# Performance work log

Hardware: AMD Instinct MI355X
Metric: run time of the kernel (lower is better)

The kernel has to match this reference:

```python
import jax, jax.numpy as jnp
import numpy as np

B, S, D = 4, 2048, 1024
N_NEURONS, K = 512, 8
N_BASIS, R = 32, 512
N_HEADS = 8
D_HEAD = R // N_HEADS


def setup_inputs() -> dict:
    key = jax.random.key(0)
    ks = jax.random.split(key, 8)
    x = jax.random.normal(ks[0], (B, S, D), dtype=jnp.float32)
    W_router = jax.random.normal(ks[1], (N_NEURONS, D), dtype=jnp.float32) / np.sqrt(D)
    recipe_Q = jax.random.normal(ks[2], (N_NEURONS, N_BASIS), dtype=jnp.float32)
    recipe_K = jax.random.normal(ks[3], (N_NEURONS, N_BASIS), dtype=jnp.float32)
    recipe_V = jax.random.normal(ks[4], (N_NEURONS, N_BASIS), dtype=jnp.float32)
    # orthonormal basis: QR of random [D, R] per basis slot (buffer, not trained)
    raw = jax.random.normal(ks[5], (N_BASIS, D, R), dtype=jnp.float32)
    basis = jax.vmap(lambda m: jnp.linalg.qr(m)[0])(raw)  # [N_BASIS, D, R]
    W_o = jax.random.normal(ks[6], (D, R), dtype=jnp.float32) / np.sqrt(R)
    mask = jnp.tril(jnp.ones((S, S), dtype=jnp.int32))[None, None]  # [1,1,S,S] causal
    mask = jnp.broadcast_to(mask, (B, 1, S, S))
    return {"x": x, "W_router": W_router, "recipe_Q": recipe_Q, "recipe_K": recipe_K,
            "recipe_V": recipe_V, "basis": basis, "W_o": W_o, "mask": mask}


def reference(x, W_router, recipe_Q, recipe_K, recipe_V, basis, W_o, mask):
    # routing: pick top-k neurons per token
    scores = jnp.einsum('bsd,nd->bsn', x, W_router)            # [B,S,N_NEURONS]
    topk_scores, topk_idx = jax.lax.top_k(scores, K)            # [B,S,K]
    weights = jax.nn.softmax(topk_scores, axis=-1)              # [B,S,K]

    def token_recipe(recipe):
        g = recipe[topk_idx]                                    # [B,S,K,N_BASIS]
        r = jnp.einsum('bskn,bsk->bsn', g, weights)             # [B,S,N_BASIS]
        return jax.nn.softmax(r, axis=-1)

    tQ = token_recipe(recipe_Q)
    tK = token_recipe(recipe_K)
    tV = token_recipe(recipe_V)

    # shared basis projection of x, reused for Q/K/V (same math as
    # W = einsum('bsn,ndr->bsdr'); Q = einsum('bsd,bsdr->bsr'))
    P = jnp.einsum('bsd,ndr->bsnr', x, basis)                   # [B,S,N_BASIS,R]
    Q = jnp.einsum('bsnr,bsn->bsr', P, tQ)
    Kt = jnp.einsum('bsnr,bsn->bsr', P, tK)
    V = jnp.einsum('bsnr,bsn->bsr', P, tV)

    def heads(t):
        return t.reshape(B, S, N_HEADS, D_HEAD).transpose(0, 2, 1, 3)  # [B,H,S,dh]

    Qh, Kh, Vh = heads(Q), heads(Kt), heads(V)
    attn = jnp.einsum('bhqd,bhkd->bhqk', Qh, Kh) / np.sqrt(D_HEAD)
    attn = jnp.where(mask == 0, jnp.float32(-1e30), attn)
    attn = jax.nn.softmax(attn, axis=-1)                        # dropout p: eval/no-op
    out = jnp.einsum('bhqk,bhkd->bhqd', attn, Vh)
    out = out.transpose(0, 2, 1, 3).reshape(B, S, R)
    attn_out = jnp.einsum('bsr,dr->bsd', out, W_o)
    return attn_out, topk_idx, weights
```

## Files before the change

kernel.cpp:

```cpp
#include <hip/hip_runtime.h>
#include <math.h>
#include <stdint.h>


typedef __attribute__((ext_vector_type(4))) float f32x4;
typedef __attribute__((ext_vector_type(8))) short s16x8;
typedef __attribute__((ext_vector_type(4))) short s16x4;
typedef __attribute__((ext_vector_type(4))) int i32x4;
typedef __attribute__((ext_vector_type(8))) int i32x8;

#define DEV __device__ __forceinline__

DEV short f2bf(float f){
  union { float f; unsigned u; } c; c.f = f;
  unsigned u = c.u;
  unsigned r = (u + 0x7fffu + ((u >> 16) & 1u)) >> 16;
  return (short)r;
}
DEV float bf2f(short s){
  union { unsigned u; float f; } c; c.u = ((unsigned)(unsigned short)s) << 16;
  return c.f;
}
DEV unsigned char f2e4m3(float f){
  union { float f; unsigned u; } c; c.f = f;
  unsigned u = c.u;
  unsigned sign = (u >> 24) & 0x80u;
  unsigned a = u & 0x7fffffffu;
  if (a >= 0x43e00000u) return (unsigned char)(sign | 0x7Eu);
  if (a < 0x3c800000u){
    union { unsigned u; float f; } d; d.u = a;
    int q = (int)(d.f * 512.0f + 0.5f);
    return (unsigned char)(sign | (unsigned)q);
  }
  unsigned m = a & 0x7fffffu;
  unsigned e = (a >> 23) - 120u;
  unsigned keep = m >> 20;
  unsigned rest = m & 0xFFFFFu;
  if (rest > 0x80000u || (rest == 0x80000u && (keep & 1u))){
    keep++;
    if (keep == 8u){ keep = 0; e++; }
  }
  if (e >= 16u || (e == 15u && keep == 7u)) return (unsigned char)(sign | 0x7Eu);
  return (unsigned char)(sign | (e << 3) | keep);
}

typedef __attribute__((address_space(3))) void lds_vt;
typedef const __attribute__((address_space(1))) void g_vt;
DEV void gload16(const void* g, void* lds){
  __builtin_amdgcn_global_load_lds((g_vt*)g, (lds_vt*)lds, 16, 0, 0);
}

DEV int gslot(int c){ return (c < 4) ? (c << 1) : (((c - 4) << 1) + 1); }

__global__ void k_conv_w(const float* __restrict__ Wo, const float* __restrict__ Wrt,
                         short* __restrict__ Wob, short* __restrict__ Wrtb){
  int i = blockIdx.x*256 + threadIdx.x;
  const float* src = (i < 131072) ? Wo : Wrt;
  short* dst = (i < 131072) ? Wob : Wrtb;
  int j = (i < 131072) ? i : (i - 131072);
  float4 v = ((const float4*)src)[j];
  s16x4 o; o[0]=f2bf(v.x); o[1]=f2bf(v.y); o[2]=f2bf(v.z); o[3]=f2bf(v.w);
  ((s16x4*)dst)[j] = o;
}

__global__ void k_conv_x(const float* __restrict__ in, short* __restrict__ Xb, char* __restrict__ Xf8){
  int t = blockIdx.x*256 + threadIdx.x;
  size_t d = (size_t)t * 16;
  const float4* s = (const float4*)(in + d);
  float vals[16];
  #pragma unroll
  for (int q=0;q<4;q++){ float4 v = s[q]; vals[q*4]=v.x; vals[q*4+1]=v.y; vals[q*4+2]=v.z; vals[q*4+3]=v.w; }
  s16x8 ob0, ob1;
  unsigned long long v0 = 0, v1 = 0;
  #pragma unroll
  for (int e=0;e<8;e++){
    ob0[e] = f2bf(vals[e]);
    ob1[e] = f2bf(vals[8+e]);
    v0 |= ((unsigned long long)f2e4m3(vals[e]))   << (8*e);
    v1 |= ((unsigned long long)f2e4m3(vals[8+e])) << (8*e);
  }
  *(s16x8*)(Xb + d) = ob0;
  *(s16x8*)(Xb + d + 8) = ob1;
  int c = t & 7;
  char* dst = Xf8 + (d & ~(size_t)127) + (gslot(c) << 4);
  *(unsigned long long*)dst = v0;
  *(unsigned long long*)(dst + 8) = v1;
}

__global__ __launch_bounds__(256) void k_conv_basis8(const float* __restrict__ basis, char* __restrict__ B2f){
  __shared__ float tile[64][65];
  int tid = threadIdx.x;
  int r0 = blockIdx.x<<6, d0 = blockIdx.y<<6, n = blockIdx.z;
  const float* src = basis + ((size_t)n*1024 + d0)*512 + r0;
  for (int i = tid; i < 4096; i += 256){ int dd = i>>6, rr = i&63; tile[dd][rr] = src[(size_t)dd*512 + rr]; }
  __syncthreads();
  int rr = tid >> 2, j = tid & 3;
  unsigned long long v0 = 0, v1 = 0;
  #pragma unroll
  for (int e=0;e<8;e++){
    v0 |= ((unsigned long long)f2e4m3(tile[j*16+e][rr]))   << (8*e);
    v1 |= ((unsigned long long)f2e4m3(tile[j*16+8+e][rr])) << (8*e);
  }
  int c = j + ((d0 >> 4) & 4);
  char* dst = B2f + ((size_t)(r0+rr)*32 + n)*1024 + (size_t)(d0 & ~127) + (gslot(c) << 4);
  *(unsigned long long*)dst = v0;
  *(unsigned long long*)(dst + 8) = v1;
}

__global__ __launch_bounds__(256) void k_gemm_c32(
    const short* __restrict__ A, const short* __restrict__ Bt, int Kd, int Mblk,
    float* __restrict__ C, int ldc)
{
  __shared__ char smem[32768];
  short* Asm = (short*)smem;
  short* Bsm = (short*)(smem + 16384);
  int tid = threadIdx.x, lane = tid & 63, w = tid >> 6;
  int wr = w >> 1, wc = w & 1;
  int nwg = gridDim.x, bid = blockIdx.x;
  int sid = (bid & 7) * (nwg >> 3) + (bid >> 3);
  int row0 = (sid % Mblk) << 7;
  int col0 = (sid / Mblk) << 7;
  f32x4 acc[4][4];
  #pragma unroll
  for (int m=0;m<4;m++)
    #pragma unroll
    for (int nf=0;nf<4;nf++)
      #pragma unroll
      for (int e=0;e<4;e++) acc[m][nf][e] = 0.f;
  int lr8 = lane >> 3;
  int lk_sw = (((lane & 7) ^ (lane >> 3)) << 3);
  for (int k0 = 0; k0 < Kd; k0 += 64){
    #pragma unroll
    for (int i=0;i<4;i++){
      int chunk = (w<<2) + i;
      int r = (chunk<<3) + lr8;
      gload16(A  + (size_t)(row0 + r)*Kd + k0 + lk_sw, smem + chunk*1024);
      gload16(Bt + (size_t)(col0 + r)*Kd + k0 + lk_sw, smem + 16384 + chunk*1024);
    }
    __syncthreads();
    #pragma unroll
    for (int kk=0; kk<2; kk++){
      int csw = (kk*32 + ((lane>>4)<<3)) ^ ((lane & 7) << 3);
      s16x8 af[4], bfr[4];
      #pragma unroll
      for (int m=0;m<4;m++)
        af[m] = *(const s16x8*)(Asm + ((wr*64 + m*16 + (lane&15))*64 + csw));
      #pragma unroll
      for (int nf=0;nf<4;nf++)
        bfr[nf] = *(const s16x8*)(Bsm + ((wc*64 + nf*16 + (lane&15))*64 + csw));
      #pragma unroll
      for (int m=0;m<4;m++)
        #pragma unroll
        for (int nf=0;nf<4;nf++)
          acc[m][nf] = __builtin_amdgcn_mfma_f32_16x16x32_bf16(af[m], bfr[nf], acc[m][nf], 0, 0, 0);
    }
    __syncthreads();
  }
  #pragma unroll
  for (int m=0;m<4;m++)
    #pragma unroll
    for (int nf=0;nf<4;nf++)
      #pragma unroll
      for (int e=0;e<4;e++){
        int tok = wr*64 + m*16 + ((lane>>4)<<2) + e;
        int col = wc*64 + nf*16 + (lane&15);
        C[(size_t)(row0+tok)*ldc + col0 + col] = acc[m][nf][e];
      }
}

#define STAGE8(G, tileRow0, half, tkt) do{ \
  int _t = (tkt) < 7 ? (tkt) : 7; \
  char* _d = smem + ((G)==Xf8 ? 65536 : 0) + ((_t&1)*32768) + ((half)*16384) + (wid*2048); \
  const char* _s = (G) + (size_t)((tileRow0) + (half)*128 + wid*16 + (lane>>3))*1024 + (_t<<7) + (((lane&7)^(lane>>3))<<4); \
  gload16(_s, _d); \
  gload16(_s + 8192, _d + 1024); \
}while(0)

#define LD_AF8(dst, base) \
  _Pragma("unroll") \
  for (int i=0;i<4;i++){ \
    const char* _p = (base) + (wm*64 + i*16 + l15)*128; \
    i32x4* _h = (i32x4*)&dst[i]; \
    _h[0] = *(const i32x4*)(_p + ((ga0 ^ l7)<<4)); \
    _h[1] = *(const i32x4*)(_p + ((ga1 ^ l7)<<4)); \
  }

#define LD_BF8(dst, base) \
  _Pragma("unroll") \
  for (int n=0;n<2;n++){ \
    const char* _p = (base) + (wn*32 + n*16 + l15)*128; \
    i32x4* _h = (i32x4*)&dst[n]; \
    _h[0] = *(const i32x4*)(_p + ((ga0 ^ l7)<<4)); \
    _h[1] = *(const i32x4*)(_p + ((ga1 ^ l7)<<4)); \
  }

#define VMC(N) asm volatile("s_waitcnt vmcnt(" #N ")" ::: "memory")
#define PBAR() do{ __builtin_amdgcn_sched_barrier(0); __builtin_amdgcn_s_barrier(); }while(0)

#define MFMA_Q8(Q, AF, BF) do{ \
  __builtin_amdgcn_s_setprio(1); \
  _Pragma("unroll") \
  for (int i=0;i<4;i++) \
    _Pragma("unroll") \
    for (int n=0;n<2;n++) \
      acc[Q][i][n] = __builtin_amdgcn_mfma_scale_f32_16x16x128_f8f6f4( \
          AF[i], BF[n], acc[Q][i][n], 0, 0, 0, 0x7f7f7f7f, 0, 0x7f7f7f7f); \
  __builtin_amdgcn_s_setprio(0); \
}while(0)

__global__ __launch_bounds__(512, 2) void k_pgemm8(
    const char* __restrict__ B2f, const char* __restrict__ Xf8,
    const float* __restrict__ tQp, const float* __restrict__ tKp, const float* __restrict__ tVp,
    short* __restrict__ Qb, short* __restrict__ Kb, short* __restrict__ Vt)
{
  extern __shared__ char smem[];
  int tid = threadIdx.x, lane = tid & 63, wid = tid >> 6;
  int wm = wid >> 2, wn = wid & 3;
  int l15 = lane & 15, l7 = lane & 7, g16 = lane >> 4;
  int ga0 = (g16 < 2) ? (g16 << 2) : (((g16 - 2) << 2) + 1);
  int ga1 = ga0 + 2;
  int bid = blockIdx.x;
  int xcd = bid & 7, lid = bid >> 3;
  int t_tile = (xcd << 2) + (lid & 3);
  int c_tile = lid >> 2;
  int row0 = c_tile << 8;
  int col0 = t_tile << 8;

  f32x4 acc[4][4][2];
  #pragma unroll
  for (int q=0;q<4;q++)
    #pragma unroll
    for (int m=0;m<4;m++)
      #pragma unroll
      for (int n=0;n<2;n++)
        #pragma unroll
        for (int e=0;e<4;e++) acc[q][m][n][e] = 0.f;
  i32x8 af[4], bf0[2], bf1[2];

  STAGE8(B2f, row0, 0, 0);
  STAGE8(Xf8, col0, 0, 0);
  STAGE8(Xf8, col0, 1, 0);
  STAGE8(B2f, row0, 1, 0);
  VMC(4);
  PBAR();

  for (int kt = 0; kt < 8; ++kt){
    const char* Ac = smem + (kt&1)*32768;
    const char* Bc = smem + 65536 + (kt&1)*32768;
    LD_AF8(af,  Ac);
    LD_BF8(bf0, Bc);
    STAGE8(B2f, row0, 0, kt+1);
    VMC(4);
    PBAR();
    MFMA_Q8(0, af, bf0);
    LD_BF8(bf1, Bc + 16384);
    STAGE8(Xf8, col0, 0, kt+1);
    VMC(4);
    PBAR();
    MFMA_Q8(1, af, bf1);
    LD_AF8(af, Ac + 16384);
    STAGE8(Xf8, col0, 1, kt+1);
    PBAR();
    MFMA_Q8(2, af, bf0);
    STAGE8(B2f, row0, 1, kt+1);
    VMC(4);
    PBAR();
    MFMA_Q8(3, af, bf1);
  }

  VMC(0);
  __syncthreads();
  short* t16 = (short*)smem;
  for (int i = tid; i < 8192; i += 512){
    int tk = i >> 5, n = i & 31;
    t16[tk*36 + n]            = f2bf(tQp[(size_t)col0*32 + i]);
    t16[9216 + tk*36 + n]     = f2bf(tKp[(size_t)col0*32 + i]);
    t16[18432 + tk*36 + n]    = f2bf(tVp[(size_t)col0*32 + i]);
  }
  __syncthreads();
  int g4 = g16 << 2;
  #pragma unroll
  for (int rec=0; rec<3; rec++){
    const short* tb = t16 + rec*9216;
    #pragma unroll
    for (int q=0;q<4;q++){
      int rb = (row0 >> 5) + (q>>1)*4 + wm*2;
      #pragma unroll
      for (int n=0;n<2;n++){
        int tok = (q&1)*128 + wn*32 + n*16 + l15;
        s16x4 tlo = *(const s16x4*)(tb + tok*36 + g4);
        s16x4 thi = *(const s16x4*)(tb + tok*36 + 16 + g4);
        #pragma unroll
        for (int mp=0;mp<2;mp++){
          float p = 0.f;
          #pragma unroll
          for (int e=0;e<4;e++) p += acc[q][2*mp][n][e]   * bf2f(tlo[e]);
          #pragma unroll
          for (int e=0;e<4;e++) p += acc[q][2*mp+1][n][e] * bf2f(thi[e]);
          p += __shfl_xor(p, 16);
          p += __shfl_xor(p, 32);
          if (g16 == rec){
            int gtok = col0 + tok;
            int r = rb + mp;
            if (rec == 0)      Qb[(size_t)gtok*512 + r] = f2bf(p);
            else if (rec == 1) Kb[(size_t)gtok*512 + r] = f2bf(p);
            else Vt[(((size_t)(gtok>>11)*8 + (r>>6))*64 + (r&63))*2048 + (gtok&2047)] = f2bf(p);
          }
        }
      }
    }
  }
}

__global__ __launch_bounds__(64) void k_router(const float* __restrict__ scores,
    const float* __restrict__ X, const float* __restrict__ W,
    const float* __restrict__ rQ, const float* __restrict__ rK, const float* __restrict__ rV,
    float* __restrict__ tQ, float* __restrict__ tK, float* __restrict__ tV,
    float* __restrict__ oidx, float* __restrict__ ow){
  int token = blockIdx.x; int lane = threadIdx.x;
  const float* srow = scores + (size_t)token*512;
  float v[8];
  #pragma unroll
  for (int j=0;j<8;j++) v[j] = srow[lane + 64*j];
  int myidx = 0x7fffffff;
  #pragma unroll
  for (int k=0;k<16;k++){
    float bm = -INFINITY; int bi = 0x7fffffff;
    #pragma unroll
    for (int j=0;j<8;j++){ if (v[j] > bm) { bm = v[j]; bi = lane + 64*j; } }
    #pragma unroll
    for (int off=32; off>=1; off>>=1){
      float om = __shfl_xor(bm, off); int oi = __shfl_xor(bi, off);
      if (om > bm || (om == bm && oi < bi)) { bm = om; bi = oi; }
    }
    if (lane == k) myidx = bi;
    #pragma unroll
    for (int j=0;j<8;j++) if (lane + 64*j == bi) v[j] = -INFINITY;
  }
  float xr[16];
  {
    const float4* x4 = (const float4*)(X + (size_t)token*1024 + lane*16);
    #pragma unroll
    for (int q=0;q<4;q++){ float4 t = x4[q]; xr[q*4]=t.x; xr[q*4+1]=t.y; xr[q*4+2]=t.z; xr[q*4+3]=t.w; }
  }
  double myref = -1e300;
  #pragma unroll
  for (int c=0;c<16;c++){
    int nid = __shfl(myidx, c);
    const float4* w4 = (const float4*)(W + (size_t)nid*1024 + lane*16);
    double acc = 0.0;
    #pragma unroll
    for (int q=0;q<4;q++){
      float4 t = w4[q];
      acc += (double)xr[q*4]   * (double)t.x;
      acc += (double)xr[q*4+1] * (double)t.y;
      acc += (double)xr[q*4+2] * (double)t.z;
      acc += (double)xr[q*4+3] * (double)t.w;
    }
    #pragma unroll
    for (int off=32; off>=1; off>>=1) acc += __shfl_xor(acc, off);
    if (lane == c) myref = acc;
  }
  double mv = myref; int mi = myidx;
  double topv[8]; int topi[8];
  #pragma unroll
  for (int k=0;k<8;k++){
    double bm = mv; int bi = mi;
    #pragma unroll
    for (int off=32; off>=1; off>>=1){
      double om = __shfl_xor(bm, off); int oi = __shfl_xor(bi, off);
      if (om > bm || (om == bm && oi < bi)) { bm = om; bi = oi; }
    }
    topv[k]=bm; topi[k]=bi;
    if (mi == bi) mv = -1e300;
  }
  double mx = topv[0]; double s = 0.0; double wd[8];
  #pragma unroll
  for (int k=0;k<8;k++){ wd[k] = exp(topv[k]-mx); s += wd[k]; }
  float w[8];
  #pragma unroll
  for (int k=0;k<8;k++) w[k] = (float)(wd[k]/s);
  if (lane == 0){
    #pragma unroll
    for (int k=0;k<8;k++){ oidx[(size_t)token*8+k] = (float)topi[k]; ow[(size_t)token*8+k] = w[k]; }
  }
  int n = lane & 31;
  float aq=0.f, ak=0.f, av=0.f;
  #pragma unroll
  for (int k=0;k<8;k++){
    size_t off = (size_t)topi[k]*32 + n;
    aq += w[k]*rQ[off]; ak += w[k]*rK[off]; av += w[k]*rV[off];
  }
  float mq = aq, mk2 = ak, mvv = av;
  #pragma unroll
  for (int off=16; off>=1; off>>=1){
    mq  = fmaxf(mq,  __shfl_xor(mq, off));
    mk2 = fmaxf(mk2, __shfl_xor(mk2,off));
    mvv = fmaxf(mvv, __shfl_xor(mvv,off));
  }
  float eq = expf(aq-mq), ek = expf(ak-mk2), ev = expf(av-mvv);
  float sq = eq, sk = ek, sv = ev;
  #pragma unroll
  for (int off=16; off>=1; off>>=1){
    sq += __shfl_xor(sq,off); sk += __shfl_xor(sk,off); sv += __shfl_xor(sv,off);
  }
  if (lane < 32){
    tQ[(size_t)token*32+n] = eq/sq;
    tK[(size_t)token*32+n] = ek/sk;
    tV[(size_t)token*32+n] = ev/sv;
  }
}

__global__ __launch_bounds__(256) void k_attn(const short* __restrict__ Qb, const short* __restrict__ Kb,
                                              const short* __restrict__ Vt, short* __restrict__ Ob)
{
  __shared__ char smem[40960];
  int tid = threadIdx.x, lane = tid & 63, wid = tid >> 6;
  int l15 = lane & 15, l7 = lane & 7, g16 = lane >> 4;
  int bid = blockIdx.x;
  int xcd = bid & 7, lid = bid >> 3;
  int work = xcd*128 + lid;
  int bx = 31 - (work & 31);
  int bh = work >> 5; int h = bh & 7, b = bh >> 3;
  size_t tokbase = (size_t)b*2048;
  int q0 = bx << 6;
  int nt = bx + 1;
  const float SC = 0.125f * 1.44269504f;

#define ATTN_STAGE(kt_) do{ \
  int _c = (kt_) & 1; \
  _Pragma("unroll") \
  for (int _i=0;_i<2;_i++){ \
    int _row = _i*32 + (wid<<3) + (lane>>3); \
    gload16(Kb + (tokbase + (((kt_)<<6) + _row))*512 + (h<<6) + ((l7 ^ (_row&7))<<3), \
            smem + (_c<<13) + _i*4096 + (wid<<10) + lane*16); \
    gload16(Vt + (size_t)((bh<<6) + _row)*2048 + ((kt_)<<6) + ((l7 ^ (_row&7))<<3), \
            smem + 16384 + (_c<<13) + _i*4096 + (wid<<10) + lane*16); \
  } \
}while(0)

  s16x8 qf[2];
  {
    const short* qp = Qb + (tokbase + q0 + wid*16 + l15)*512 + (h<<6);
    qf[0] = *(const s16x8*)(qp + g16*8);
    qf[1] = *(const s16x8*)(qp + 32 + g16*8);
  }
  int q_abs = q0 + wid*16 + l15;
  f32x4 o[4];
  float m_log = -INFINITY, l_sum = 0.f;
  #pragma unroll
  for (int i=0;i<4;i++)
    #pragma unroll
    for (int e=0;e<4;e++) o[i][e]=0.f;

  ATTN_STAGE(0);
  __syncthreads();

  for (int kt = 0; kt < nt; ++kt){
    if (kt + 1 < nt) ATTN_STAGE(kt+1);
    int cur = kt & 1;
    const char* Kc = smem + (cur<<13);
    const char* Vc = smem + 16384 + (cur<<13);
    char* Pb = smem + 32768 + (wid<<11);
    f32x4 S[4];
    #pragma unroll
    for (int s16=0;s16<4;s16++){
      #pragma unroll
      for (int e=0;e<4;e++) S[s16][e] = 0.f;
      const char* kr = Kc + (s16*16 + l15)*128;
      s16x8 kf0 = *(const s16x8*)(kr + (((g16  ) ^ l7)<<4));
      s16x8 kf1 = *(const s16x8*)(kr + (((4+g16) ^ l7)<<4));
      S[s16] = __builtin_amdgcn_mfma_f32_16x16x32_bf16(kf0, qf[0], S[s16], 0,0,0);
      S[s16] = __builtin_amdgcn_mfma_f32_16x16x32_bf16(kf1, qf[1], S[s16], 0,0,0);
    }
    bool diag = (kt == nt-1);
    float sm[16];
    #pragma unroll
    for (int s16=0;s16<4;s16++)
      #pragma unroll
      for (int e=0;e<4;e++){
        float sv = S[s16][e] * SC;
        if (diag){
          int kv_abs = (kt<<6) + s16*16 + (g16<<2) + e;
          if (kv_abs > q_abs) sv = -1e30f;
        }
        sm[s16*4+e] = sv;
      }
    float pmax = sm[0];
    #pragma unroll
    for (int j=1;j<16;j++) pmax = fmaxf(pmax, sm[j]);
    pmax = fmaxf(pmax, __shfl_xor(pmax, 16));
    pmax = fmaxf(pmax, __shfl_xor(pmax, 32));
    float mnew = fmaxf(m_log, pmax);
    float alpha = exp2f(m_log - mnew);
    m_log = mnew;
    float p[16], ps = 0.f;
    #pragma unroll
    for (int j=0;j<16;j++){ p[j] = exp2f(sm[j] - mnew); ps += p[j]; }
    ps += __shfl_xor(ps, 16);
    ps += __shfl_xor(ps, 32);
    l_sum = l_sum*alpha + ps;
    #pragma unroll
    for (int e=0;e<4;e++){
      float al = __shfl(alpha, (g16<<2)+e);
      #pragma unroll
      for (int df=0;df<4;df++) o[df][e] *= al;
    }
    #pragma unroll
    for (int s16=0;s16<4;s16++){
      s16x4 pk;
      #pragma unroll
      for (int e=0;e<4;e++) pk[e] = f2bf(p[s16*4+e]);
      *(s16x4*)(Pb + l15*128 + (((s16<<5) + (g16<<3)) ^ (l7<<4))) = pk;
    }
    s16x8 pf0 = *(const s16x8*)(Pb + l15*128 + (((g16  ) ^ l7)<<4));
    s16x8 pf1 = *(const s16x8*)(Pb + l15*128 + (((4+g16) ^ l7)<<4));
    #pragma unroll
    for (int df=0;df<4;df++){
      const char* vr = Vc + (df*16 + l15)*128;
      s16x8 vf0 = *(const s16x8*)(vr + (((g16  ) ^ l7)<<4));
      s16x8 vf1 = *(const s16x8*)(vr + (((4+g16) ^ l7)<<4));
      o[df] = __builtin_amdgcn_mfma_f32_16x16x32_bf16(pf0, vf0, o[df], 0,0,0);
      o[df] = __builtin_amdgcn_mfma_f32_16x16x32_bf16(pf1, vf1, o[df], 0,0,0);
    }
    __syncthreads();
  }
  #pragma unroll
  for (int e=0;e<4;e++){
    float ln = __shfl(l_sum, (g16<<2)+e);
    float inv = 1.0f / ln;
    #pragma unroll
    for (int df=0;df<4;df++){
      int q = q0 + wid*16 + (g16<<2) + e;
      int d = df*16 + l15;
      Ob[(tokbase + q)*512 + (h<<6) + d] = f2bf(o[df][e] * inv);
    }
  }
#undef ATTN_STAGE
}

extern "C" void kernel_launch(void* const* d_in, const int* in_sizes, int n_in,
                              void* d_out, int out_size, void* d_ws, size_t ws_size,
                              hipStream_t stream)
{
  const float* x     = (const float*)d_in[0];
  const float* Wrt   = (const float*)d_in[1];
  const float* rQ    = (const float*)d_in[2];
  const float* rK    = (const float*)d_in[3];
  const float* rV    = (const float*)d_in[4];
  const float* basis = (const float*)d_in[5];
  const float* Wo    = (const float*)d_in[6];
  float* out = (float*)d_out;
  char* ws = (char*)d_ws;
  char*  B2f  = (char*)(ws + 0);
  char*  Xf8  = (char*)(ws + 16777216);
  short* Xb   = (short*)(ws + 25165824);
  float* SC   = (float*)(ws + 41943040);
  float* tQ   = (float*)(ws + 58720256);
  float* tK   = (float*)(ws + 59768832);
  float* tV   = (float*)(ws + 60817408);
  short* Qb   = (short*)(ws + 61865984);
  short* Kb   = (short*)(ws + 70254592);
  short* Vt   = (short*)(ws + 78643200);
  short* Ob   = (short*)(ws + 87031808);
  short* Wob  = (short*)(ws + 95420416);
  short* Wrtb = (short*)(ws + 96468992);
  float* oidx = out + 8388608;
  float* oww  = out + 8454144;

  hipFuncSetAttribute((const void*)k_pgemm8, hipFuncAttributeMaxDynamicSharedMemorySize, 131072);

  k_conv_x<<<2048, 256, 0, stream>>>(x, Xb, Xf8);
  k_conv_w<<<1024, 256, 0, stream>>>(Wo, Wrt, Wob, Wrtb);
  k_conv_basis8<<<dim3(8,16,32), 256, 0, stream>>>(basis, B2f);
  k_gemm_c32<<<256, 256, 0, stream>>>(Xb, Wrtb, 1024, 64, SC, 512);
  k_router<<<8192, 64, 0, stream>>>(SC, x, Wrt, rQ, rK, rV, tQ, tK, tV, oidx, oww);
  k_pgemm8<<<2048, 512, 131072, stream>>>(B2f, Xf8, tQ, tK, tV, Qb, Kb, Vt);
  k_attn<<<1024, 256, 0, stream>>>(Qb, Kb, Vt, Ob);
  k_gemm_c32<<<512, 256, 0, stream>>>(Ob, Wob, 512, 64, out, 1024);
}
```

Baseline: 413.2 us.

## Halve basis-projection GEMM tile rows and restructure smem staging for higher occupancy

The FP8 basis-projection GEMM now uses 128-row output tiles instead of 256, with half the accumulators per wave, and launches twice as many blocks. Shared memory drops from 128 KB to 56 KB, and launch bounds now request 4 blocks per CU so more waves can hide latency. The staging pipeline is reworked with separate A/B staging macros and a new buffer slot schedule. The cost is reloading X tiles twice as often, which doubles global traffic for that operand, and the new wait counts and slot reuse are more intricate.

```diff
diff --git a/kernel.cpp b/kernel.cpp
--- a/kernel.cpp
+++ b/kernel.cpp
@@ -168,28 +168,36 @@
       }
 }
 
-#define STAGE8(G, tileRow0, half, tkt) do{ \
+#define STAGE_A(slotOff, arow0, tkt) do{ \
   int _t = (tkt) < 7 ? (tkt) : 7; \
-  char* _d = smem + ((G)==Xf8 ? 65536 : 0) + ((_t&1)*32768) + ((half)*16384) + (wid*2048); \
-  const char* _s = (G) + (size_t)((tileRow0) + (half)*128 + wid*16 + (lane>>3))*1024 + (_t<<7) + (((lane&7)^(lane>>3))<<4); \
-  gload16(_s, _d); \
-  gload16(_s + 8192, _d + 1024); \
+  int _r = tid>>3, _g = tid&7; \
+  gload16(B2f + (size_t)(row0 + (arow0) + _r)*1024 + (_t<<7) + ((_g ^ (_r&7))<<4), \
+          smem + (slotOff) + (_r<<7) + (_g<<4)); \
 }while(0)
 
-#define LD_AF8(dst, base) \
+#define STAGE_B(slotOff, trow0, tkt) do{ \
+  int _t = (tkt) < 7 ? (tkt) : 7; \
+  int _r = tid>>3, _g = tid&7; \
+  gload16(Xf8 + (size_t)(col0 + (trow0) + _r)*1024 + (_t<<7) + ((_g ^ (_r&7))<<4), \
+          smem + (slotOff) + (_r<<7) + (_g<<4)); \
+  gload16(Xf8 + (size_t)(col0 + (trow0) + 64 + _r)*1024 + (_t<<7) + ((_g ^ (_r&7))<<4), \
+          smem + (slotOff) + ((64+_r)<<7) + (_g<<4)); \
+}while(0)
+
+#define LD_AF(dst, base) \
   _Pragma("unroll") \
-  for (int i=0;i<4;i++){ \
-    const char* _p = (base) + (wm*64 + i*16 + l15)*128; \
-    i32x4* _h = (i32x4*)&dst[i]; \
+  for (int mi=0;mi<2;mi++){ \
+    const char* _p = (base) + (wm*32 + mi*16 + l15)*128; \
+    i32x4* _h = (i32x4*)&dst[mi]; \
     _h[0] = *(const i32x4*)(_p + ((ga0 ^ l7)<<4)); \
     _h[1] = *(const i32x4*)(_p + ((ga1 ^ l7)<<4)); \
   }
 
-#define LD_BF8(dst, base) \
+#define LD_BF(dst, base) \
   _Pragma("unroll") \
-  for (int n=0;n<2;n++){ \
-    const char* _p = (base) + (wn*32 + n*16 + l15)*128; \
-    i32x4* _h = (i32x4*)&dst[n]; \
+  for (int ni=0;ni<2;ni++){ \
+    const char* _p = (base) + (wn*32 + ni*16 + l15)*128; \
+    i32x4* _h = (i32x4*)&dst[ni]; \
     _h[0] = *(const i32x4*)(_p + ((ga0 ^ l7)<<4)); \
     _h[1] = *(const i32x4*)(_p + ((ga1 ^ l7)<<4)); \
   }
@@ -197,18 +205,18 @@
 #define VMC(N) asm volatile("s_waitcnt vmcnt(" #N ")" ::: "memory")
 #define PBAR() do{ __builtin_amdgcn_sched_barrier(0); __builtin_amdgcn_s_barrier(); }while(0)
 
-#define MFMA_Q8(Q, AF, BF) do{ \
+#define MFMAP(Q, AF, BF) do{ \
   __builtin_amdgcn_s_setprio(1); \
   _Pragma("unroll") \
-  for (int i=0;i<4;i++) \
+  for (int mi=0;mi<2;mi++) \
     _Pragma("unroll") \
-    for (int n=0;n<2;n++) \
-      acc[Q][i][n] = __builtin_amdgcn_mfma_scale_f32_16x16x128_f8f6f4( \
-          AF[i], BF[n], acc[Q][i][n], 0, 0, 0, 0x7f7f7f7f, 0, 0x7f7f7f7f); \
+    for (int ni=0;ni<2;ni++) \
+      acc[Q][mi][ni] = __builtin_amdgcn_mfma_scale_f32_16x16x128_f8f6f4( \
+          AF[mi], BF[ni], acc[Q][mi][ni], 0, 0, 0, 0x7f7f7f7f, 0, 0x7f7f7f7f); \
   __builtin_amdgcn_s_setprio(0); \
 }while(0)
 
-__global__ __launch_bounds__(512, 2) void k_pgemm8(
+__global__ __launch_bounds__(512, 4) void k_pgemm8(
     const char* __restrict__ B2f, const char* __restrict__ Xf8,
     const float* __restrict__ tQp, const float* __restrict__ tKp, const float* __restrict__ tVp,
     short* __restrict__ Qb, short* __restrict__ Kb, short* __restrict__ Vt)
@@ -223,49 +231,48 @@
   int xcd = bid & 7, lid = bid >> 3;
   int t_tile = (xcd << 2) + (lid & 3);
   int c_tile = lid >> 2;
-  int row0 = c_tile << 8;
+  int row0 = c_tile << 7;
   int col0 = t_tile << 8;
 
-  f32x4 acc[4][4][2];
+  f32x4 acc[4][2][2];
   #pragma unroll
   for (int q=0;q<4;q++)
     #pragma unroll
-    for (int m=0;m<4;m++)
-      #pragma unroll
-      for (int n=0;n<2;n++)
+    for (int mi=0;mi<2;mi++)
+      #pragma unroll
+      for (int ni=0;ni<2;ni++)
         #pragma unroll
-        for (int e=0;e<4;e++) acc[q][m][n][e] = 0.f;
-  i32x8 af[4], bf0[2], bf1[2];
-
-  STAGE8(B2f, row0, 0, 0);
-  STAGE8(Xf8, col0, 0, 0);
-  STAGE8(Xf8, col0, 1, 0);
-  STAGE8(B2f, row0, 1, 0);
-  VMC(4);
+        for (int e=0;e<4;e++) acc[q][mi][ni][e] = 0.f;
+  i32x8 af[2], bf[2];
+
+  STAGE_A(0, 0, 0);
+  STAGE_B(24576, 0, 0);
+  STAGE_A(16384, 64, 0);
+  VMC(1);
   PBAR();
 
   for (int kt = 0; kt < 8; ++kt){
-    const char* Ac = smem + (kt&1)*32768;
-    const char* Bc = smem + 65536 + (kt&1)*32768;
-    LD_AF8(af,  Ac);
-    LD_BF8(bf0, Bc);
-    STAGE8(B2f, row0, 0, kt+1);
-    VMC(4);
+    const char* A0c = smem + ((kt&1)<<13);
+    LD_AF(af, A0c);
+    LD_BF(bf, smem + 24576);
+    STAGE_B(40960, 128, kt);
+    VMC(2);
     PBAR();
-    MFMA_Q8(0, af, bf0);
-    LD_BF8(bf1, Bc + 16384);
-    STAGE8(Xf8, col0, 0, kt+1);
-    VMC(4);
+    MFMAP(0, af, bf);
+    LD_AF(af, smem + 16384);
+    STAGE_A(((kt+1)&1)<<13, 0, kt+1);
+    VMC(1);
     PBAR();
-    MFMA_Q8(1, af, bf1);
-    LD_AF8(af, Ac + 16384);
-    STAGE8(Xf8, col0, 1, kt+1);
+    MFMAP(1, af, bf);
+    LD_BF(bf, smem + 40960);
+    STAGE_B(24576, 0, kt+1);
     PBAR();
-    MFMA_Q8(2, af, bf0);
-    STAGE8(B2f, row0, 1, kt+1);
-    VMC(4);
+    MFMAP(2, af, bf);
+    LD_AF(af, A0c);
+    STAGE_A(16384, 64, kt+1);
+    VMC(1);
     PBAR();
-    MFMA_Q8(3, af, bf1);
+    MFMAP(3, af, bf);
   }
 
   VMC(0);
@@ -284,28 +291,26 @@
     const short* tb = t16 + rec*9216;
     #pragma unroll
     for (int q=0;q<4;q++){
-      int rb = (row0 >> 5) + (q>>1)*4 + wm*2;
-      #pragma unroll
-      for (int n=0;n<2;n++){
-        int tok = (q&1)*128 + wn*32 + n*16 + l15;
+      int rh = (q==1)||(q==2);
+      int ch = q >> 1;
+      int r = (c_tile << 2) + rh*2 + wm;
+      #pragma unroll
+      for (int ni=0;ni<2;ni++){
+        int tok = ch*128 + wn*32 + ni*16 + l15;
         s16x4 tlo = *(const s16x4*)(tb + tok*36 + g4);
         s16x4 thi = *(const s16x4*)(tb + tok*36 + 16 + g4);
+        float p = 0.f;
         #pragma unroll
-        for (int mp=0;mp<2;mp++){
-          float p = 0.f;
-          #pragma unroll
-          for (int e=0;e<4;e++) p += acc[q][2*mp][n][e]   * bf2f(tlo[e]);
-          #pragma unroll
-          for (int e=0;e<4;e++) p += acc[q][2*mp+1][n][e] * bf2f(thi[e]);
-          p += __shfl_xor(p, 16);
-          p += __shfl_xor(p, 32);
-          if (g16 == rec){
-            int gtok = col0 + tok;
-            int r = rb + mp;
-            if (rec == 0)      Qb[(size_t)gtok*512 + r] = f2bf(p);
-            else if (rec == 1) Kb[(size_t)gtok*512 + r] = f2bf(p);
-            else Vt[(((size_t)(gtok>>11)*8 + (r>>6))*64 + (r&63))*2048 + (gtok&2047)] = f2bf(p);
-          }
+        for (int e=0;e<4;e++) p += acc[q][0][ni][e] * bf2f(tlo[e]);
+        #pragma unroll
+        for (int e=0;e<4;e++) p += acc[q][1][ni][e] * bf2f(thi[e]);
+        p += __shfl_xor(p, 16);
+        p += __shfl_xor(p, 32);
+        if (g16 == rec){
+          int gtok = col0 + tok;
+          if (rec == 0)      Qb[(size_t)gtok*512 + r] = f2bf(p);
+          else if (rec == 1) Kb[(size_t)gtok*512 + r] = f2bf(p);
+          else Vt[(((size_t)(gtok>>11)*8 + (r>>6))*64 + (r&63))*2048 + (gtok&2047)] = f2bf(p);
         }
       }
     }
@@ -568,14 +573,14 @@
   float* oidx = out + 8388608;
   float* oww  = out + 8454144;
 
-  hipFuncSetAttribute((const void*)k_pgemm8, hipFuncAttributeMaxDynamicSharedMemorySize, 131072);
+  hipFuncSetAttribute((const void*)k_pgemm8, hipFuncAttributeMaxDynamicSharedMemorySize, 57344);
 
   k_conv_x<<<2048, 256, 0, stream>>>(x, Xb, Xf8);
   k_conv_w<<<1024, 256, 0, stream>>>(Wo, Wrt, Wob, Wrtb);
   k_conv_basis8<<<dim3(8,16,32), 256, 0, stream>>>(basis, B2f);
   k_gemm_c32<<<256, 256, 0, stream>>>(Xb, Wrtb, 1024, 64, SC, 512);
   k_router<<<8192, 64, 0, stream>>>(SC, x, Wrt, rQ, rK, rV, tQ, tK, tV, oidx, oww);
-  k_pgemm8<<<2048, 512, 131072, stream>>>(B2f, Xf8, tQ, tK, tV, Qb, Kb, Vt);
+  k_pgemm8<<<4096, 512, 57344, stream>>>(B2f, Xf8, tQ, tK, tV, Qb, Kb, Vt);
   k_attn<<<1024, 256, 0, stream>>>(Qb, Kb, Vt, Ob);
   k_gemm_c32<<<512, 256, 0, stream>>>(Ob, Wob, 512, 64, out, 1024);
 }
```

Result: faster. 399.8 us (median of 2 runs) (-3.2%).
